# Kernel tuning notes

Measured on AMD Instinct MI355X. Metric: run time of the kernel, lower is better.

Reference implementation:

```python
import jax, jax.numpy as jnp
import numpy as np

N, D_IN, D_LAT, D_FEAT, K = 12000, 64, 16, 64, 16


def setup_inputs() -> dict:
    key = jax.random.key(0)
    ks = jax.random.split(key, 7)
    s_in = 1.0 / np.sqrt(D_IN)
    s_cat = 1.0 / np.sqrt(2 * D_FEAT)
    return {
        "x": jax.random.normal(ks[0], (N, D_IN), dtype=jnp.float32),
        "W_feat": jax.random.uniform(ks[1], (D_IN, D_FEAT), jnp.float32, -s_in, s_in),
        "b_feat": jax.random.uniform(ks[2], (D_FEAT,), jnp.float32, -s_in, s_in),
        "W_lat": jax.random.uniform(ks[3], (D_IN, D_LAT), jnp.float32, -s_in, s_in),
        "b_lat": jax.random.uniform(ks[4], (D_LAT,), jnp.float32, -s_in, s_in),
        "W_out": jax.random.uniform(ks[5], (2 * D_FEAT, D_FEAT), jnp.float32, -s_cat, s_cat),
        "b_out": jax.random.uniform(ks[6], (D_FEAT,), jnp.float32, -s_cat, s_cat),
    }


def reference(x, W_feat, b_feat, W_lat, b_lat, W_out, b_out):
    # dense encoders
    feats = jnp.tanh(x @ W_feat + b_feat)      # [N, F] learned features
    coords = jnp.tanh(x @ W_lat + b_lat)       # [N, S] latent coordinates
    n = coords.shape[0]
    # full pairwise squared euclidean distances (as the module's cdist)
    sq = jnp.sum(coords * coords, axis=1)
    d2 = sq[:, None] + sq[None, :] - 2.0 * (coords @ coords.T)   # [N, N]
    d2 = jnp.maximum(d2, 0.0)
    # knn_graph: k nearest neighbors, excluding self (loop=False)
    d2_masked = jnp.where(jnp.eye(n, dtype=bool), jnp.inf, d2)
    neg_d2, idx = jax.lax.top_k(-d2_masked, K)                   # idx: [N, K] neighbor (source) ids
    edge_d2 = -neg_d2                                            # squared dist to each neighbor
    # gaussian kernel on euclidean distance: w = exp(-d^2)
    w = jnp.exp(-edge_d2)                                        # [N, K]
    # message = w * x_j, aggr='add': out_i = sum_k w_ik * feats[idx_ik]
    agg = jnp.einsum('nk,nkf->nf', w, feats[idx])                # [N, F]
    # cat self features with aggregated messages, final dense
    out = jnp.concatenate([feats, agg], axis=1) @ W_out + b_out  # [N, F]
    return out
```

## Files before the change

### kernel.cpp

```cpp
#include <hip/hip_runtime.h>
#include <math.h>

typedef unsigned long long u64;
typedef _Float16 f16x8 __attribute__((ext_vector_type(8)));
typedef float f32x4 __attribute__((ext_vector_type(4)));

#define N_PTS 12000
#define KNN 16
#define QB 16
#define NWAVES 8
#define NGROUPS (N_PTS / 16)
#define TAU_PTS 2048
#define TAU_GROUPS (TAU_PTS / 16)
#define CAP 384
#define MARGIN 0.08f

__global__ __launch_bounds__(256) void encoder_kernel(
    const float* __restrict__ x, const float* __restrict__ Wf, const float* __restrict__ bf,
    const float* __restrict__ Wl, const float* __restrict__ bl,
    float* __restrict__ feats, float* __restrict__ coords, _Float16* __restrict__ coords_h,
    float* __restrict__ sq)
{
  const int wave = threadIdx.x >> 6;
  const int lane = threadIdx.x & 63;
  const int i = blockIdx.x * 4 + wave;
  if (i >= N_PTS) return;
  float xv = x[i * 64 + lane];
  float accf = bf[lane];
  float accc = bl[lane & 15];
  #pragma unroll
  for (int k = 0; k < 64; ++k) {
    float xk = __shfl(xv, k);
    accf = fmaf(xk, Wf[k * 64 + lane], accf);
    accc = fmaf(xk, Wl[k * 16 + (lane & 15)], accc);
  }
  feats[i * 64 + lane] = tanhf(accf);
  float c = tanhf(accc);
  float cc = (lane < 16) ? c * c : 0.0f;
  cc += __shfl_xor(cc, 1);
  cc += __shfl_xor(cc, 2);
  cc += __shfl_xor(cc, 4);
  cc += __shfl_xor(cc, 8);
  if (lane < 16) {
    coords[i * 16 + lane] = c;
    coords_h[i * 16 + lane] = (_Float16)c;
  }
  if (lane == 0) sq[i] = cc;
}

__device__ __forceinline__ void ins6(u64 key, u64* k6, u64& kmax) {
  const u64 om = (key < kmax) ? kmax : ~0ull;
  #pragma unroll
  for (int t = 0; t < 6; ++t)
    k6[t] = (k6[t] == om) ? key : k6[t];
  u64 a = k6[0] > k6[1] ? k6[0] : k6[1];
  u64 b = k6[2] > k6[3] ? k6[2] : k6[3];
  u64 c = k6[4] > k6[5] ? k6[4] : k6[5];
  a = a > b ? a : b;
  kmax = a > c ? a : c;
}

__device__ __forceinline__ void ins8(u64 key, u64* k8, u64& kmax) {
  const u64 om = (key < kmax) ? kmax : ~0ull;
  #pragma unroll
  for (int t = 0; t < 8; ++t)
    k8[t] = (k8[t] == om) ? key : k8[t];
  u64 a = k8[0] > k8[1] ? k8[0] : k8[1];
  u64 b = k8[2] > k8[3] ? k8[2] : k8[3];
  u64 c = k8[4] > k8[5] ? k8[4] : k8[5];
  u64 d = k8[6] > k8[7] ? k8[6] : k8[7];
  a = a > b ? a : b;
  c = c > d ? c : d;
  kmax = a > c ? a : c;
}

__device__ __forceinline__ u64 shflx_u64(u64 v, int off) {
  int lo = __shfl_xor((int)(unsigned)v, off);
  int hi = __shfl_xor((int)(unsigned)(v >> 32), off);
  return ((u64)(unsigned)hi << 32) | (unsigned)lo;
}

__device__ __forceinline__ u64 minbfly(u64 m) {
  #pragma unroll
  for (int off = 32; off >= 1; off >>= 1) {
    u64 o = shflx_u64(m, off);
    m = (o < m) ? o : m;
  }
  return m;
}

__global__ __launch_bounds__(512) void knn_agg_kernel(
    const float* __restrict__ coords, const _Float16* __restrict__ coords_h,
    const float* __restrict__ sq, const float* __restrict__ feats,
    const float* __restrict__ Wo, const float* __restrict__ bo,
    float* __restrict__ out, int* __restrict__ flags)
{
  __shared__ unsigned short sbuf[QB][CAP];
  __shared__ int scnt[QB];
  __shared__ float colminS[QB][NWAVES * 16];
  __shared__ float taugS[QB];
  __shared__ float featS[QB][64];
  __shared__ float aggS[QB][64];

  const int tid = threadIdx.x;
  const int lane = tid & 63;
  const int wave = tid >> 6;
  const int qbase = blockIdx.x * QB;
  const int n = lane & 15;
  const int quad = lane >> 4;

  if (tid < QB) scnt[tid] = 0;

  f16x8 afrag = {0, 0, 0, 0, 0, 0, 0, 0};
  if (lane < 32) {
    const uint4 u = *(const uint4*)((const char*)coords_h + (qbase + n) * 32 + quad * 16);
    afrag = __builtin_bit_cast(f16x8, u);
  }
  const float4 sqi4v = *(const float4*)&sq[qbase + quad * 4];
  const float sqi4[4] = {sqi4v.x, sqi4v.y, sqi4v.z, sqi4v.w};

  __syncthreads();

  float lmin4[4] = {INFINITY, INFINITY, INFINITY, INFINITY};
  for (int g = wave; g < TAU_GROUPS; g += NWAVES) {
    const int j0 = g * 16;
    f16x8 bfrag = {0, 0, 0, 0, 0, 0, 0, 0};
    if (lane < 32) {
      const uint4 u = *(const uint4*)((const char*)coords_h + (j0 + n) * 32 + quad * 16);
      bfrag = __builtin_bit_cast(f16x8, u);
    }
    const float sqj = sq[j0 + n];
    f32x4 acc = {0.0f, 0.0f, 0.0f, 0.0f};
    acc = __builtin_amdgcn_mfma_f32_16x16x32_f16(afrag, bfrag, acc, 0, 0, 0);
    #pragma unroll
    for (int r = 0; r < 4; ++r) {
      float d2a = fmaf(-2.0f, acc[r], sqi4[r] + sqj);
      if (j0 + n == qbase + quad * 4 + r) d2a = INFINITY;
      lmin4[r] = fminf(lmin4[r], d2a);
    }
  }
  #pragma unroll
  for (int r = 0; r < 4; ++r)
    colminS[quad * 4 + r][wave * 16 + n] = lmin4[r];
  __syncthreads();

  #pragma unroll
  for (int s = 0; s < 2; ++s) {
    const int q = wave * 2 + s;
    float v = fminf(colminS[q][lane], colminS[q][64 + lane]);
    #pragma unroll
    for (int k = 2; k <= 64; k <<= 1) {
      #pragma unroll
      for (int st = k >> 1; st >= 1; st >>= 1) {
        const float o = __shfl_xor(v, st);
        const bool keepMin = (((lane & st) == 0) == ((lane & k) == 0));
        const float mn = fminf(v, o), mx = fmaxf(v, o);
        v = keepMin ? mn : mx;
      }
    }
    const float tq = __shfl(v, 15) + MARGIN;
    if (lane == 0) taugS[q] = tq;
  }
  __syncthreads();

  float taug4[4];
  #pragma unroll
  for (int r = 0; r < 4; ++r) taug4[r] = taugS[quad * 4 + r];

  for (int g = wave; g < NGROUPS; g += NWAVES) {
    const int j0 = g * 16;
    f16x8 bfrag = {0, 0, 0, 0, 0, 0, 0, 0};
    if (lane < 32) {
      const uint4 u = *(const uint4*)((const char*)coords_h + (j0 + n) * 32 + quad * 16);
      bfrag = __builtin_bit_cast(f16x8, u);
    }
    const float sqj = sq[j0 + n];
    f32x4 acc = {0.0f, 0.0f, 0.0f, 0.0f};
    acc = __builtin_amdgcn_mfma_f32_16x16x32_f16(afrag, bfrag, acc, 0, 0, 0);
    #pragma unroll
    for (int r = 0; r < 4; ++r) {
      const float d2a = fmaf(-2.0f, acc[r], sqi4[r] + sqj);
      if (d2a <= taug4[r]) {
        const int row = quad * 4 + r;
        const int p = atomicAdd(&scnt[row], 1);
        if (p < CAP) sbuf[row][p] = (unsigned short)(j0 + n);
      }
    }
  }
  __syncthreads();

  #pragma unroll
  for (int s = 0; s < 2; ++s) {
    const int lq = wave * 2 + s;
    const int qg = qbase + lq;
    const int cq = scnt[lq];
    const int nread = (cq < CAP) ? cq : CAP;

    float ci[16];
    {
      const float4* cp = (const float4*)(coords + qg * 16);
      *(float4*)&ci[0] = cp[0]; *(float4*)&ci[4] = cp[1];
      *(float4*)&ci[8] = cp[2]; *(float4*)&ci[12] = cp[3];
    }
    const float sqiq = sq[qg];

    u64 k6[6];
    #pragma unroll
    for (int t = 0; t < 6; ++t) k6[t] = ((u64)(0x7F000000u + t) << 32);
    u64 kmax6 = ((u64)0x7F000005u << 32);

    #pragma unroll
    for (int t = 0; t < CAP / 64; ++t) {
      const int idx = t * 64 + lane;
      u64 key = ~0ull;
      if (idx < nread) {
        const int jj = sbuf[lq][idx];
        if (jj != qg) {
          const float4* cp = (const float4*)(coords + jj * 16);
          float cj[16];
          *(float4*)&cj[0]  = cp[0]; *(float4*)&cj[4]  = cp[1];
          *(float4*)&cj[8]  = cp[2]; *(float4*)&cj[12] = cp[3];
          float dot = 0.0f;
          #pragma unroll
          for (int d = 0; d < 16; ++d) dot = fmaf(ci[d], cj[d], dot);
          const float d2 = fmaxf(fmaf(-2.0f, dot, sqiq + sq[jj]), 0.0f);
          key = ((u64)__float_as_uint(d2) << 32) | (unsigned)jj;
        }
      }
      ins6(key, k6, kmax6);
    }

    u64 lmin = k6[0];
    #pragma unroll
    for (int t = 1; t < 6; ++t) lmin = (k6[t] < lmin) ? k6[t] : lmin;

    float aggv = 0.0f;
    for (int r = 0; r < KNN; ++r) {
      const u64 m = minbfly(lmin);
      if (lmin == m) {
        #pragma unroll
        for (int t = 0; t < 6; ++t) k6[t] = (k6[t] == m) ? ~0ull : k6[t];
        lmin = k6[0];
        #pragma unroll
        for (int t = 1; t < 6; ++t) lmin = (k6[t] < lmin) ? k6[t] : lmin;
      }
      const unsigned hi = (unsigned)(m >> 32);
      const bool ok = hi < 0x7F000000u;
      const float w = ok ? expf(-__uint_as_float(hi)) : 0.0f;
      const int jj = ok ? (int)(unsigned)(m & 0xFFFFFFFFull) : 0;
      aggv = fmaf(w, feats[jj * 64 + lane], aggv);
    }
    aggS[lq][lane] = aggv;
    featS[lq][lane] = feats[qg * 64 + lane];
    if (lane == 0) flags[qg] = (cq > CAP);
  }

  __syncthreads();
  const int row = tid >> 5;
  const int c0 = tid & 31;
  float acc0 = bo[c0], acc1 = bo[c0 + 32];
  #pragma unroll
  for (int f = 0; f < 64; ++f) {
    const float fv = featS[row][f];
    const float av = aggS[row][f];
    acc0 = fmaf(fv, Wo[f * 64 + c0],        acc0);
    acc1 = fmaf(fv, Wo[f * 64 + c0 + 32],   acc1);
    acc0 = fmaf(av, Wo[(64 + f) * 64 + c0],      acc0);
    acc1 = fmaf(av, Wo[(64 + f) * 64 + c0 + 32], acc1);
  }
  const int orow = qbase + row;
  out[orow * 64 + c0]      = acc0;
  out[orow * 64 + c0 + 32] = acc1;
}

__global__ __launch_bounds__(256) void knn_fixup_kernel(
    const float* __restrict__ coords, const float* __restrict__ sq,
    const float* __restrict__ feats, const int* __restrict__ flags,
    const float* __restrict__ Wo, const float* __restrict__ bo,
    float* __restrict__ out)
{
  const int wave = threadIdx.x >> 6;
  const int lane = threadIdx.x & 63;
  const int i = blockIdx.x * 4 + wave;
  if (i >= N_PTS) return;
  if (!flags[i]) return;
  float ci[16];
  #pragma unroll
  for (int d = 0; d < 16; ++d) ci[d] = coords[i * 16 + d];
  const float sqi = sq[i];

  u64 k8a[8], k8b[8], kmaxA, kmaxB;
  #pragma unroll
  for (int t = 0; t < 8; ++t) {
    k8a[t] = ((u64)(0x7F000000u + t) << 32);
    k8b[t] = ((u64)(0x7F000000u + t) << 32);
  }
  kmaxA = ((u64)0x7F000007u << 32);
  kmaxB = ((u64)0x7F000007u << 32);

  const int niter = (N_PTS + 63) / 64;
  for (int t = 0; t < niter; ++t) {
    const int j = t * 64 + lane;
    float4 c0 = make_float4(0,0,0,0), c1 = c0, c2 = c0, c3 = c0;
    float sqj = 0.0f;
    if (j < N_PTS) {
      const float4* cp = (const float4*)(coords + j * 16);
      c0 = cp[0]; c1 = cp[1]; c2 = cp[2]; c3 = cp[3];
      sqj = sq[j];
    }
    float dot = ci[0]*c0.x + ci[1]*c0.y + ci[2]*c0.z + ci[3]*c0.w
              + ci[4]*c1.x + ci[5]*c1.y + ci[6]*c1.z + ci[7]*c1.w
              + ci[8]*c2.x + ci[9]*c2.y + ci[10]*c2.z + ci[11]*c2.w
              + ci[12]*c3.x + ci[13]*c3.y + ci[14]*c3.z + ci[15]*c3.w;
    float d2 = fmaxf(fmaf(-2.0f, dot, sqi + sqj), 0.0f);
    const unsigned hi = (j == i || j >= N_PTS) ? 0xFFFFFFFFu : __float_as_uint(d2);
    const u64 key = ((u64)hi << 32) | (unsigned)j;
    if (t & 1) ins8(key, k8a, kmaxA);
    else       ins8(key, k8b, kmaxB);
  }

  u64 tab[16];
  #pragma unroll
  for (int t = 0; t < 8; ++t) { tab[t] = k8a[t]; tab[8 + t] = k8b[t]; }
  u64 lmin = tab[0];
  #pragma unroll
  for (int t = 1; t < 16; ++t) lmin = (tab[t] < lmin) ? tab[t] : lmin;

  float aggv = 0.0f;
  u64 T16 = 0;
  for (int r = 0; r < KNN; ++r) {
    const u64 m = minbfly(lmin);
    if (lmin == m) {
      #pragma unroll
      for (int t = 0; t < 16; ++t) tab[t] = (tab[t] == m) ? ~0ull : tab[t];
      lmin = tab[0];
      #pragma unroll
      for (int t = 1; t < 16; ++t) lmin = (tab[t] < lmin) ? tab[t] : lmin;
    }
    const unsigned hi = (unsigned)(m >> 32);
    const bool ok = hi < 0x7F000000u;
    const float w = ok ? expf(-__uint_as_float(hi)) : 0.0f;
    const int jj = ok ? (int)(unsigned)(m & 0xFFFFFFFFull) : 0;
    aggv = fmaf(w, feats[jj * 64 + lane], aggv);
    T16 = m;
  }

  if (__any((kmaxA < T16) || (kmaxB < T16))) {
    aggv = 0.0f;
    u64 prev = 0;
    for (int r = 0; r < KNN; ++r) {
      u64 best = ~0ull;
      for (int j = lane; j < N_PTS; j += 64) {
        float dot = 0.0f;
        #pragma unroll
        for (int d = 0; d < 16; ++d) dot = fmaf(ci[d], coords[j * 16 + d], dot);
        const float d2 = fmaxf(fmaf(-2.0f, dot, sqi + sq[j]), 0.0f);
        const unsigned hi = (j == i) ? 0xFFFFFFFFu : __float_as_uint(d2);
        const u64 key = ((u64)hi << 32) | (unsigned)j;
        const bool cand = (r == 0) || (key > prev);
        if (cand && key < best) best = key;
      }
      const u64 m = minbfly(best);
      prev = m;
      const unsigned hi = (unsigned)(m >> 32);
      const bool ok = hi < 0x7F000000u;
      const float w = ok ? expf(-__uint_as_float(hi)) : 0.0f;
      const int jj = ok ? (int)(unsigned)(m & 0xFFFFFFFFull) : 0;
      aggv = fmaf(w, feats[jj * 64 + lane], aggv);
    }
  }

  const float fl = feats[i * 64 + lane];
  float acc = bo[lane];
  #pragma unroll
  for (int f = 0; f < 64; ++f) {
    acc = fmaf(__shfl(fl, f),   Wo[f * 64 + lane],        acc);
    acc = fmaf(__shfl(aggv, f), Wo[(64 + f) * 64 + lane], acc);
  }
  out[i * 64 + lane] = acc;
}

extern "C" void kernel_launch(void* const* d_in, const int* in_sizes, int n_in,
                              void* d_out, int out_size, void* d_ws, size_t ws_size,
                              hipStream_t stream) {
  const float* x  = (const float*)d_in[0];
  const float* Wf = (const float*)d_in[1];
  const float* bf = (const float*)d_in[2];
  const float* Wl = (const float*)d_in[3];
  const float* bl = (const float*)d_in[4];
  const float* Wo = (const float*)d_in[5];
  const float* bo = (const float*)d_in[6];
  float* out = (float*)d_out;

  char* ws = (char*)d_ws;
  float*     feats    = (float*)(ws);
  float*     coords   = (float*)(ws + 3072000);
  float*     sqv      = (float*)(ws + 3840000);
  _Float16*  coords_h = (_Float16*)(ws + 3888000);
  int*       flags    = (int*)(ws + 4272000);

  encoder_kernel<<<3000, 256, 0, stream>>>(x, Wf, bf, Wl, bl, feats, coords, coords_h, sqv);
  knn_agg_kernel<<<N_PTS / QB, 512, 0, stream>>>(coords, coords_h, sqv, feats, Wo, bo, out, flags);
  knn_fixup_kernel<<<3000, 256, 0, stream>>>(coords, sqv, feats, flags, Wo, bo, out);
}
```

Measured before the change: 187.9 us.

## Switch distance MFMA from 16x16x32 to 32x32x16 with 32-column tiles

Replaces the 16x16x32 f16 MFMA with a 32x32x16 MFMA, so each instruction scores 16 query rows against 32 candidate points and all 64 lanes load B fragments. Only half of the A rows hold queries; the rest are zero, which wastes half the MFMA output and leaves 8 accumulators per lane in use. This halves the loop trip count for both the threshold and candidate-collection passes. The threshold column-min reduction now goes through shared-memory atomicMin on float bits instead of direct stores, which adds LDS atomic traffic and contention.

```diff
diff --git a/kernel.cpp b/kernel.cpp
--- a/kernel.cpp
+++ b/kernel.cpp
@@ -3,15 +3,15 @@
 
 typedef unsigned long long u64;
 typedef _Float16 f16x8 __attribute__((ext_vector_type(8)));
-typedef float f32x4 __attribute__((ext_vector_type(4)));
+typedef float f32x16 __attribute__((ext_vector_type(16)));
 
 #define N_PTS 12000
 #define KNN 16
 #define QB 16
 #define NWAVES 8
-#define NGROUPS (N_PTS / 16)
+#define NGROUPS32 (N_PTS / 32)
 #define TAU_PTS 2048
-#define TAU_GROUPS (TAU_PTS / 16)
+#define TAU_GROUPS32 (TAU_PTS / 32)
 #define CAP 384
 #define MARGIN 0.08f
 
@@ -97,7 +97,7 @@
 {
   __shared__ unsigned short sbuf[QB][CAP];
   __shared__ int scnt[QB];
-  __shared__ float colminS[QB][NWAVES * 16];
+  __shared__ unsigned colminS[QB][64];
   __shared__ float taugS[QB];
   __shared__ float featS[QB][64];
   __shared__ float aggS[QB][64];
@@ -106,48 +106,59 @@
   const int lane = tid & 63;
   const int wave = tid >> 6;
   const int qbase = blockIdx.x * QB;
-  const int n = lane & 15;
-  const int quad = lane >> 4;
+  const int mcol = lane & 31;
+  const int half = lane >> 5;
 
   if (tid < QB) scnt[tid] = 0;
+  #pragma unroll
+  for (int t = tid; t < QB * 64; t += 512)
+    ((unsigned*)colminS)[t] = 0x7F800000u;
 
   f16x8 afrag = {0, 0, 0, 0, 0, 0, 0, 0};
-  if (lane < 32) {
-    const uint4 u = *(const uint4*)((const char*)coords_h + (qbase + n) * 32 + quad * 16);
+  if (mcol < QB) {
+    const uint4 u = *(const uint4*)((const char*)coords_h + (qbase + mcol) * 32 + half * 16);
     afrag = __builtin_bit_cast(f16x8, u);
   }
-  const float4 sqi4v = *(const float4*)&sq[qbase + quad * 4];
-  const float sqi4[4] = {sqi4v.x, sqi4v.y, sqi4v.z, sqi4v.w};
-
+  float sqi8[8];
+  #pragma unroll
+  for (int blk = 0; blk < 2; ++blk) {
+    const float4 v = *(const float4*)&sq[qbase + blk * 8 + 4 * half];
+    sqi8[blk * 4 + 0] = v.x; sqi8[blk * 4 + 1] = v.y;
+    sqi8[blk * 4 + 2] = v.z; sqi8[blk * 4 + 3] = v.w;
+  }
   __syncthreads();
 
-  float lmin4[4] = {INFINITY, INFINITY, INFINITY, INFINITY};
-  for (int g = wave; g < TAU_GROUPS; g += NWAVES) {
-    const int j0 = g * 16;
-    f16x8 bfrag = {0, 0, 0, 0, 0, 0, 0, 0};
-    if (lane < 32) {
-      const uint4 u = *(const uint4*)((const char*)coords_h + (j0 + n) * 32 + quad * 16);
-      bfrag = __builtin_bit_cast(f16x8, u);
-    }
-    const float sqj = sq[j0 + n];
-    f32x4 acc = {0.0f, 0.0f, 0.0f, 0.0f};
-    acc = __builtin_amdgcn_mfma_f32_16x16x32_f16(afrag, bfrag, acc, 0, 0, 0);
-    #pragma unroll
-    for (int r = 0; r < 4; ++r) {
-      float d2a = fmaf(-2.0f, acc[r], sqi4[r] + sqj);
-      if (j0 + n == qbase + quad * 4 + r) d2a = INFINITY;
-      lmin4[r] = fminf(lmin4[r], d2a);
-    }
-  }
-  #pragma unroll
-  for (int r = 0; r < 4; ++r)
-    colminS[quad * 4 + r][wave * 16 + n] = lmin4[r];
+  float lmin8[8] = {INFINITY, INFINITY, INFINITY, INFINITY,
+                    INFINITY, INFINITY, INFINITY, INFINITY};
+  for (int g = wave; g < TAU_GROUPS32; g += NWAVES) {
+    const int j0 = g * 32;
+    const uint4 u = *(const uint4*)((const char*)coords_h + (j0 + mcol) * 32 + half * 16);
+    const f16x8 bfrag = __builtin_bit_cast(f16x8, u);
+    const float sqj = sq[j0 + mcol];
+    f32x16 acc = {0.0f};
+    acc = __builtin_amdgcn_mfma_f32_32x32x16_f16(afrag, bfrag, acc, 0, 0, 0);
+    #pragma unroll
+    for (int r = 0; r < 8; ++r) {
+      const int row = (r >> 2) * 8 + 4 * half + (r & 3);
+      float d2a = fmaf(-2.0f, acc[r], sqi8[r] + sqj);
+      if (j0 + mcol == qbase + row) d2a = INFINITY;
+      lmin8[r] = fminf(lmin8[r], d2a);
+    }
+  }
+  {
+    const int cell = mcol * 2 + (wave >> 2);
+    #pragma unroll
+    for (int r = 0; r < 8; ++r) {
+      const int row = (r >> 2) * 8 + 4 * half + (r & 3);
+      atomicMin(&colminS[row][cell], __float_as_uint(fmaxf(lmin8[r], 0.0f)));
+    }
+  }
   __syncthreads();
 
   #pragma unroll
   for (int s = 0; s < 2; ++s) {
     const int q = wave * 2 + s;
-    float v = fminf(colminS[q][lane], colminS[q][64 + lane]);
+    float v = __uint_as_float(colminS[q][lane]);
     #pragma unroll
     for (int k = 2; k <= 64; k <<= 1) {
       #pragma unroll
@@ -163,27 +174,25 @@
   }
   __syncthreads();
 
-  float taug4[4];
-  #pragma unroll
-  for (int r = 0; r < 4; ++r) taug4[r] = taugS[quad * 4 + r];
-
-  for (int g = wave; g < NGROUPS; g += NWAVES) {
-    const int j0 = g * 16;
-    f16x8 bfrag = {0, 0, 0, 0, 0, 0, 0, 0};
-    if (lane < 32) {
-      const uint4 u = *(const uint4*)((const char*)coords_h + (j0 + n) * 32 + quad * 16);
-      bfrag = __builtin_bit_cast(f16x8, u);
-    }
-    const float sqj = sq[j0 + n];
-    f32x4 acc = {0.0f, 0.0f, 0.0f, 0.0f};
-    acc = __builtin_amdgcn_mfma_f32_16x16x32_f16(afrag, bfrag, acc, 0, 0, 0);
-    #pragma unroll
-    for (int r = 0; r < 4; ++r) {
-      const float d2a = fmaf(-2.0f, acc[r], sqi4[r] + sqj);
-      if (d2a <= taug4[r]) {
-        const int row = quad * 4 + r;
+  float taug8[8];
+  #pragma unroll
+  for (int r = 0; r < 8; ++r)
+    taug8[r] = taugS[(r >> 2) * 8 + 4 * half + (r & 3)];
+
+  for (int g = wave; g < NGROUPS32; g += NWAVES) {
+    const int j0 = g * 32;
+    const uint4 u = *(const uint4*)((const char*)coords_h + (j0 + mcol) * 32 + half * 16);
+    const f16x8 bfrag = __builtin_bit_cast(f16x8, u);
+    const float sqj = sq[j0 + mcol];
+    f32x16 acc = {0.0f};
+    acc = __builtin_amdgcn_mfma_f32_32x32x16_f16(afrag, bfrag, acc, 0, 0, 0);
+    #pragma unroll
+    for (int r = 0; r < 8; ++r) {
+      const float d2a = fmaf(-2.0f, acc[r], sqi8[r] + sqj);
+      if (d2a <= taug8[r]) {
+        const int row = (r >> 2) * 8 + 4 * half + (r & 3);
         const int p = atomicAdd(&scnt[row], 1);
-        if (p < CAP) sbuf[row][p] = (unsigned short)(j0 + n);
+        if (p < CAP) sbuf[row][p] = (unsigned short)(j0 + mcol);
       }
     }
   }
```

Result: faster. 174.7 us (-7.0%).
